# Kernel optimization log

Measured on AMD Instinct MI355X. Metric: run time of the kernel, lower is better.

## Reference

```python
import jax, jax.numpy as jnp
import numpy as np

OUT_F, IN_F = 8192, 4096
TOKENS = 512


def _unpack_int2_to_ternary(packed, alpha, dtype):
    # packed: [out_f, in_f//4] ints 0..255; 4 two-bit codes per byte.
    # code 0 -> -1, code 2 -> +1, codes 1/3 -> 0; then scale by per-row alpha.
    shifts = jnp.arange(4, dtype=packed.dtype) * 2  # [0,2,4,6]
    two_bit = (packed[:, :, None] >> shifts[None, None, :]) & 3  # [out_f, in_f//4, 4]
    two_bit = two_bit.reshape(packed.shape[0], -1)  # [out_f, in_f]
    sign = jnp.where(two_bit == 2, 1.0, jnp.where(two_bit == 0, -1.0, 0.0)).astype(dtype)
    return sign * alpha.astype(dtype)[:, None]


def setup_inputs() -> dict:
    key = jax.random.key(0)
    k1, k2, k3, k4 = jax.random.split(key, 4)
    x = jax.random.normal(k1, (TOKENS, IN_F), dtype=jnp.float32)
    weight_int2 = jax.random.randint(k2, (OUT_F, IN_F // 4), 0, 256, dtype=jnp.int32)
    alpha = jax.random.uniform(k3, (OUT_F,), dtype=jnp.float32, minval=0.01, maxval=0.05)
    bias = jax.random.normal(k4, (OUT_F,), dtype=jnp.float32) * 0.01
    return {"x": x, "weight_int2": weight_int2, "alpha": alpha, "bias": bias}


def reference(x, weight_int2, alpha, bias):
    W = _unpack_int2_to_ternary(weight_int2, alpha, x.dtype)  # [out_f, in_f]
    out = x @ W.T  # [tokens, out_f]
    return out + bias
```

## Files before the change

### kernel.cpp

```cpp
#include <hip/hip_runtime.h>
#include <hip/hip_bf16.h>

typedef unsigned int u32;
typedef unsigned short u16;

#define TOKENS 512
#define OUT_F  8192
#define IN_F   4096
#define KPACK  (IN_F / 4)
#define NSTEP  64

typedef __attribute__((ext_vector_type(8))) short bf16x8;
typedef __attribute__((ext_vector_type(4))) float f32x4;
typedef __attribute__((ext_vector_type(16))) float f32x16;

__device__ __forceinline__ u32 pack_bf16x2(float a, float b) {
    __hip_bfloat162 h = __float22bfloat162_rn(make_float2(a, b));
    union { __hip_bfloat162 h2; u32 u; } cvt;
    cvt.h2 = h;
    return cvt.u;
}

__device__ __forceinline__ void decode4(u32 b, u32& lo, u32& hi) {
    u32 t = b + (b << 14);
    u32 u = t >> 4;
    u32 nt = ~t, nu = ~u;
    lo = __umul24(nt & 0x10001u, 0x3F80u) | ((nt & 0x20002u) << 14);
    hi = __umul24(nu & 0x10001u, 0x3F80u) | ((nu & 0x20002u) << 14);
}

__device__ __forceinline__ bf16x8 decode_frag(u32 hw) {
    u32 d0, d1, d2, d3;
    decode4(hw & 0xFFu, d0, d1);
    decode4((hw >> 8) & 0xFFu, d2, d3);
    union { bf16x8 v; u32 u[4]; } c;
    c.u[0] = d0; c.u[1] = d1; c.u[2] = d2; c.u[3] = d3;
    return c.v;
}

__device__ __forceinline__ void async_ld16(const void* g, void* l) {
    __builtin_amdgcn_global_load_lds(
        (const __attribute__((address_space(1))) u32*)g,
        (__attribute__((address_space(3))) u32*)l, 16, 0, 0);
}

__global__ __launch_bounds__(256) void convert_x(const float* __restrict__ X,
                                                 u16* __restrict__ Xb) {
    int i = (blockIdx.x * 256 + threadIdx.x) * 8;
    float4 a = *(const float4*)(X + i);
    float4 b = *(const float4*)(X + i + 4);
    uint4 q;
    q.x = pack_bf16x2(a.x, a.y);
    q.y = pack_bf16x2(a.z, a.w);
    q.z = pack_bf16x2(b.x, b.y);
    q.w = pack_bf16x2(b.z, b.w);
    *(uint4*)(Xb + i) = q;
}

__global__ __launch_bounds__(256) void repack_w6(const u32* __restrict__ W2,
                                                 u32* __restrict__ W6) {
    __shared__ u32 staged[128 * 16];
    const int ngrp = blockIdx.x;
    const int kc   = blockIdx.y;
    const int t = threadIdx.x;

    {
        const int c = t & 15;
#pragma unroll
        for (int i = 0; i < 8; ++i) {
            int r = i * 16 + (t >> 4);
            uint4 w = *(const uint4*)(W2 + (size_t)(ngrp * 128 + r) * KPACK + kc * 64 + c * 4);
            staged[r * 16 + (c ^ (r & 15))] =
                (w.x & 0xFFu) | ((w.y & 0xFFu) << 8) | ((w.z & 0xFFu) << 16) | ((w.w & 0xFFu) << 24);
        }
    }
    __syncthreads();
    {
        const u16* sp = (const u16*)staged;
#pragma unroll
        for (int j = 0; j < 8; ++j) {
            int e = t + 256 * j;
            int lane = e & 63;
            int kq   = (e >> 6) & 3;
            int Sl   = (e >> 8) & 3;
            int nh   = (e >> 10) & 1;
            int hw = Sl * 8 + kq * 2 + (lane >> 5);
            int r0 = nh * 64 + (lane & 31);
            int r1 = r0 + 32;
            u32 x0 = sp[r0 * 32 + 2 * ((hw >> 1) ^ (r0 & 15)) + (hw & 1)];
            u32 x1 = sp[r1 * 32 + 2 * ((hw >> 1) ^ (r1 & 15)) + (hw & 1)];
            size_t idx = (size_t)(ngrp * 2 + nh) * 16384 + (size_t)(kc * 4 + Sl) * 256
                       + kq * 64 + lane;
            W6[idx] = x0 | (x1 << 16);
        }
    }
}

__global__ __launch_bounds__(512, 2) void ternary_gemm_ks(
    const u16* __restrict__ Xb,
    const u32* __restrict__ W6,
    const float* __restrict__ alpha,
    const float* __restrict__ bias,
    float* __restrict__ Out)
{
    __shared__ uint4 smem[4096];
    u16* As = (u16*)smem;

    const int tid  = threadIdx.x;
    const int lane = tid & 63;
    const int wave = tid >> 6;
    const int kq = wave & 3;
    const int nh = wave >> 2;

    const int m0 = blockIdx.x * 128;
    const int n0 = blockIdx.y * 128;
    const int ngrp = blockIdx.y;

    f32x16 acc[4][2];
#pragma unroll
    for (int mt = 0; mt < 4; ++mt)
#pragma unroll
        for (int nt = 0; nt < 2; ++nt)
#pragma unroll
            for (int i = 0; i < 16; ++i)
                acc[mt][nt][i] = 0.f;

    const int slot = ((kq * 2 + (lane >> 5)) ^ (lane & 7));
    int ofsA[4];
#pragma unroll
    for (int mt = 0; mt < 4; ++mt)
        ofsA[mt] = (mt * 32 + (lane & 31)) * 64 + slot * 8;

    const int r_l = lane >> 3;
    const int c_l = (lane & 7) ^ r_l;
    const u16* gA[2];
    u16* lA[2];
#pragma unroll
    for (int i = 0; i < 2; ++i) {
        int rbase = wave * 16 + i * 8;
        gA[i] = Xb + (size_t)(m0 + rbase + r_l) * IN_F + c_l * 8;
        lA[i] = As + rbase * 64;
    }

    const u32* wp = W6 + (size_t)(ngrp * 2 + nh) * 16384 + kq * 64 + lane;

    u32 wcur = wp[0];
    u32 wnxt = wp[256];
#pragma unroll
    for (int i = 0; i < 2; ++i) async_ld16(gA[i], lA[i]);
    __syncthreads();

    for (int s = 0; s < NSTEP; ++s) {
        const int buf = s & 1;
        if (s + 1 < NSTEP) {
            const int off = (s + 1) * 64;
#pragma unroll
            for (int i = 0; i < 2; ++i)
                async_ld16(gA[i] + off, lA[i] + (buf ^ 1) * 8192);
        }
        u32 wtmp = 0;
        if (s + 2 < NSTEP) wtmp = wp[(size_t)(s + 2) * 256];

        const u16* ab = As + buf * 8192;
        bf16x8 a0 = *(const bf16x8*)(ab + ofsA[0]);
        bf16x8 a1 = *(const bf16x8*)(ab + ofsA[1]);
        bf16x8 a2 = *(const bf16x8*)(ab + ofsA[2]);
        bf16x8 a3 = *(const bf16x8*)(ab + ofsA[3]);
        bf16x8 b0 = decode_frag(wcur & 0xFFFFu);
        bf16x8 b1 = decode_frag(wcur >> 16);

        acc[0][0] = __builtin_amdgcn_mfma_f32_32x32x16_bf16(a0, b0, acc[0][0], 0, 0, 0);
        acc[1][0] = __builtin_amdgcn_mfma_f32_32x32x16_bf16(a1, b0, acc[1][0], 0, 0, 0);
        acc[2][0] = __builtin_amdgcn_mfma_f32_32x32x16_bf16(a2, b0, acc[2][0], 0, 0, 0);
        acc[3][0] = __builtin_amdgcn_mfma_f32_32x32x16_bf16(a3, b0, acc[3][0], 0, 0, 0);
        acc[0][1] = __builtin_amdgcn_mfma_f32_32x32x16_bf16(a0, b1, acc[0][1], 0, 0, 0);
        acc[1][1] = __builtin_amdgcn_mfma_f32_32x32x16_bf16(a1, b1, acc[1][1], 0, 0, 0);
        acc[2][1] = __builtin_amdgcn_mfma_f32_32x32x16_bf16(a2, b1, acc[2][1], 0, 0, 0);
        acc[3][1] = __builtin_amdgcn_mfma_f32_32x32x16_bf16(a3, b1, acc[3][1], 0, 0, 0);

        wcur = wnxt;
        wnxt = wtmp;
        __syncthreads();
    }

    f32x4* red = (f32x4*)smem;
#pragma unroll 1
    for (int q = 1; q < 4; ++q) {
        if (kq == q) {
            f32x4* dst = red + nh * 2048 + lane;
#pragma unroll
            for (int mt = 0; mt < 4; ++mt)
#pragma unroll
                for (int nt = 0; nt < 2; ++nt)
#pragma unroll
                    for (int sub = 0; sub < 4; ++sub) {
                        f32x4 v = {acc[mt][nt][sub * 4 + 0], acc[mt][nt][sub * 4 + 1],
                                   acc[mt][nt][sub * 4 + 2], acc[mt][nt][sub * 4 + 3]};
                        dst[(mt * 8 + nt * 4 + sub) * 64] = v;
                    }
        }
        __syncthreads();
        if (kq == 0) {
            const f32x4* src = red + nh * 2048 + lane;
#pragma unroll
            for (int mt = 0; mt < 4; ++mt)
#pragma unroll
                for (int nt = 0; nt < 2; ++nt)
#pragma unroll
                    for (int sub = 0; sub < 4; ++sub) {
                        f32x4 v = src[(mt * 8 + nt * 4 + sub) * 64];
#pragma unroll
                        for (int i = 0; i < 4; ++i)
                            acc[mt][nt][sub * 4 + i] += v[i];
                    }
        }
        __syncthreads();
    }

    if (kq == 0) {
#pragma unroll
        for (int nt = 0; nt < 2; ++nt) {
            int ncol = n0 + nh * 64 + nt * 32 + (lane & 31);
            float av = alpha[ncol];
            float bv = bias[ncol];
#pragma unroll
            for (int mt = 0; mt < 4; ++mt) {
#pragma unroll
                for (int r = 0; r < 16; ++r) {
                    int row = m0 + mt * 32 + (r & 3) + 8 * (r >> 2) + 4 * (lane >> 5);
                    Out[(size_t)row * OUT_F + ncol] = acc[mt][nt][r] * av + bv;
                }
            }
        }
    }
}

__global__ void ternary_naive(const float* __restrict__ X, const u32* __restrict__ W2,
                              const float* __restrict__ alpha, const float* __restrict__ bias,
                              float* __restrict__ Out) {
    int o  = blockIdx.x * 64 + (threadIdx.x & 63);
    int tk = blockIdx.y * 4 + (threadIdx.x >> 6);
    const float* x = X + (size_t)tk * IN_F;
    const u32* w = W2 + (size_t)o * KPACK;
    float s = 0.f;
    for (int d = 0; d < KPACK; ++d) {
        u32 b = w[d] & 0xFFu;
        const float* xp = x + d * 4;
#pragma unroll
        for (int j = 0; j < 4; ++j) {
            u32 c = (b >> (2 * j)) & 3u;
            float wv = (c == 2u) ? 1.f : ((c == 0u) ? -1.f : 0.f);
            s += xp[j] * wv;
        }
    }
    Out[(size_t)tk * OUT_F + o] = s * alpha[o] + bias[o];
}

extern "C" void kernel_launch(void* const* d_in, const int* in_sizes, int n_in,
                              void* d_out, int out_size, void* d_ws, size_t ws_size,
                              hipStream_t stream) {
    const float* x = (const float*)d_in[0];
    const u32* w2 = (const u32*)d_in[1];
    const float* alpha = (const float*)d_in[2];
    const float* bias  = (const float*)d_in[3];
    float* out = (float*)d_out;

    const size_t xb_bytes = (size_t)TOKENS * IN_F * sizeof(u16);
    const size_t w6_bytes = (size_t)OUT_F * IN_F / 4;

    if (ws_size >= xb_bytes + w6_bytes) {
        u16* xb = (u16*)d_ws;
        u32* w6 = (u32*)((char*)d_ws + xb_bytes);
        convert_x<<<(TOKENS * IN_F) / (256 * 8), 256, 0, stream>>>(x, xb);
        repack_w6<<<dim3(64, 16), 256, 0, stream>>>(w2, w6);
        ternary_gemm_ks<<<dim3(4, 64), 512, 0, stream>>>(xb, w6, alpha, bias, out);
    } else {
        ternary_naive<<<dim3(OUT_F / 64, TOKENS / 4), 256, 0, stream>>>(x, w2, alpha, bias, out);
    }
}
```

Before: 137.6 us.

## Shrink M tile to 64, widen K window to 128, and use a cheaper perm-based ternary decode

Result: faster. 131.8 us (-4.2%).

```diff
diff --git a/kernel.cpp b/kernel.cpp
--- a/kernel.cpp
+++ b/kernel.cpp
@@ -8,7 +8,10 @@
 #define OUT_F  8192
 #define IN_F   4096
 #define KPACK  (IN_F / 4)
-#define NSTEP  64
+#define TM 64
+#define TN 128
+#define BKW 128
+#define NWIN (IN_F / BKW)
 
 typedef __attribute__((ext_vector_type(8))) short bf16x8;
 typedef __attribute__((ext_vector_type(4))) float f32x4;
@@ -21,20 +24,16 @@
     return cvt.u;
 }
 
-__device__ __forceinline__ void decode4(u32 b, u32& lo, u32& hi) {
-    u32 t = b + (b << 14);
-    u32 u = t >> 4;
-    u32 nt = ~t, nu = ~u;
-    lo = __umul24(nt & 0x10001u, 0x3F80u) | ((nt & 0x20002u) << 14);
-    hi = __umul24(nu & 0x10001u, 0x3F80u) | ((nu & 0x20002u) << 14);
-}
-
-__device__ __forceinline__ bf16x8 decode_frag(u32 hw) {
-    u32 d0, d1, d2, d3;
-    decode4(hw & 0xFFu, d0, d1);
-    decode4((hw >> 8) & 0xFFu, d2, d3);
+__device__ __forceinline__ u32 decode_pair(u32 d) {
+    u32 s = (__umul24(d, 0x808202u) & 0x06060606u) + 0x01000100u;
+    return __builtin_amdgcn_perm(0x00003F80u, 0x0000BF80u, s);
+}
+__device__ __forceinline__ bf16x8 decode_frag(u32 w, int sh) {
     union { bf16x8 v; u32 u[4]; } c;
-    c.u[0] = d0; c.u[1] = d1; c.u[2] = d2; c.u[3] = d3;
+    c.u[0] = decode_pair((w >> (sh + 0)) & 0xFu);
+    c.u[1] = decode_pair((w >> (sh + 4)) & 0xFu);
+    c.u[2] = decode_pair((w >> (sh + 8)) & 0xFu);
+    c.u[3] = decode_pair((w >> (sh + 12)) & 0xFu);
     return c.v;
 }
 
@@ -57,54 +56,52 @@
     *(uint4*)(Xb + i) = q;
 }
 
-__global__ __launch_bounds__(256) void repack_w6(const u32* __restrict__ W2,
-                                                 u32* __restrict__ W6) {
-    __shared__ u32 staged[128 * 16];
+__global__ __launch_bounds__(256) void repack_w7(const u32* __restrict__ W2,
+                                                 uint2* __restrict__ W7) {
+    __shared__ u32 dense[128 * 32];
     const int ngrp = blockIdx.x;
     const int kc   = blockIdx.y;
     const int t = threadIdx.x;
-
-    {
-        const int c = t & 15;
-#pragma unroll
-        for (int i = 0; i < 8; ++i) {
-            int r = i * 16 + (t >> 4);
-            uint4 w = *(const uint4*)(W2 + (size_t)(ngrp * 128 + r) * KPACK + kc * 64 + c * 4);
-            staged[r * 16 + (c ^ (r & 15))] =
-                (w.x & 0xFFu) | ((w.y & 0xFFu) << 8) | ((w.z & 0xFFu) << 16) | ((w.w & 0xFFu) << 24);
-        }
+#pragma unroll
+    for (int i = 0; i < 16; ++i) {
+        int id = t + 256 * i;
+        int col = id >> 5, jq = id & 31;
+        uint4 wv = *(const uint4*)(W2 + (size_t)(ngrp * 128 + col) * KPACK + kc * 128 + jq * 4);
+        dense[col * 32 + (jq ^ (col & 31))] =
+            (wv.x & 0xFFu) | ((wv.y & 0xFFu) << 8) | ((wv.z & 0xFFu) << 16) | ((wv.w & 0xFFu) << 24);
     }
     __syncthreads();
-    {
-        const u16* sp = (const u16*)staged;
-#pragma unroll
-        for (int j = 0; j < 8; ++j) {
-            int e = t + 256 * j;
-            int lane = e & 63;
-            int kq   = (e >> 6) & 3;
-            int Sl   = (e >> 8) & 3;
-            int nh   = (e >> 10) & 1;
-            int hw = Sl * 8 + kq * 2 + (lane >> 5);
-            int r0 = nh * 64 + (lane & 31);
-            int r1 = r0 + 32;
-            u32 x0 = sp[r0 * 32 + 2 * ((hw >> 1) ^ (r0 & 15)) + (hw & 1)];
-            u32 x1 = sp[r1 * 32 + 2 * ((hw >> 1) ^ (r1 & 15)) + (hw & 1)];
-            size_t idx = (size_t)(ngrp * 2 + nh) * 16384 + (size_t)(kc * 4 + Sl) * 256
-                       + kq * 64 + lane;
-            W6[idx] = x0 | (x1 << 16);
-        }
-    }
-}
-
-__global__ __launch_bounds__(512, 2) void ternary_gemm_ks(
+    const u16* sp = (const u16*)dense;
+#pragma unroll
+    for (int p = 0; p < 8; ++p) {
+        int e = t + 256 * p;
+        int lane = e & 63;
+        int kq = (e >> 6) & 3;
+        int wloc = (e >> 8) & 3;
+        int nh = (e >> 10) & 1;
+        int h = lane >> 5;
+        int c0 = nh * 64 + (lane & 31), c1 = c0 + 32;
+        int j0 = wloc * 8 + kq * 2;
+        u32 x0 = sp[((c0 * 32 + (j0 ^ (c0 & 31))) << 1) | h];
+        u32 x1 = sp[((c0 * 32 + ((j0 + 1) ^ (c0 & 31))) << 1) | h];
+        u32 y0 = sp[((c1 * 32 + (j0 ^ (c1 & 31))) << 1) | h];
+        u32 y1 = sp[((c1 * 32 + ((j0 + 1) ^ (c1 & 31))) << 1) | h];
+        uint2 o;
+        o.x = x0 | (x1 << 16);
+        o.y = y0 | (y1 << 16);
+        int w = kc * 4 + wloc;
+        W7[(((size_t)(ngrp * 2 + nh) * 32 + w) * 4 + kq) * 64 + lane] = o;
+    }
+}
+
+__global__ __launch_bounds__(512, 4) void ternary_gemm7(
     const u16* __restrict__ Xb,
-    const u32* __restrict__ W6,
+    const uint2* __restrict__ W7,
     const float* __restrict__ alpha,
     const float* __restrict__ bias,
     float* __restrict__ Out)
 {
-    __shared__ uint4 smem[4096];
-    u16* As = (u16*)smem;
+    __shared__ u16 As[2][TM * BKW];
 
     const int tid  = threadIdx.x;
     const int lane = tid & 63;
@@ -112,103 +109,103 @@
     const int kq = wave & 3;
     const int nh = wave >> 2;
 
-    const int m0 = blockIdx.x * 128;
-    const int n0 = blockIdx.y * 128;
-    const int ngrp = blockIdx.y;
-
-    f32x16 acc[4][2];
-#pragma unroll
-    for (int mt = 0; mt < 4; ++mt)
+    const int id = blockIdx.x;
+    const int m0 = (id & 7) * TM;
+    const int ngrp = id >> 3;
+    const int n0 = ngrp * TN;
+
+    f32x16 acc[2][2];
+#pragma unroll
+    for (int mt = 0; mt < 2; ++mt)
 #pragma unroll
         for (int nt = 0; nt < 2; ++nt)
 #pragma unroll
             for (int i = 0; i < 16; ++i)
                 acc[mt][nt][i] = 0.f;
 
-    const int slot = ((kq * 2 + (lane >> 5)) ^ (lane & 7));
-    int ofsA[4];
-#pragma unroll
-    for (int mt = 0; mt < 4; ++mt)
-        ofsA[mt] = (mt * 32 + (lane & 31)) * 64 + slot * 8;
-
-    const int r_l = lane >> 3;
-    const int c_l = (lane & 7) ^ r_l;
-    const u16* gA[2];
-    u16* lA[2];
+    const u16* ga[2];
+    u32 lbase[2];
 #pragma unroll
     for (int i = 0; i < 2; ++i) {
-        int rbase = wave * 16 + i * 8;
-        gA[i] = Xb + (size_t)(m0 + rbase + r_l) * IN_F + c_l * 8;
-        lA[i] = As + rbase * 64;
-    }
-
-    const u32* wp = W6 + (size_t)(ngrp * 2 + nh) * 16384 + kq * 64 + lane;
-
-    u32 wcur = wp[0];
-    u32 wnxt = wp[256];
-#pragma unroll
-    for (int i = 0; i < 2; ++i) async_ld16(gA[i], lA[i]);
+        int rbase = wave * 8 + i * 4;
+        int row = rbase + (lane >> 4);
+        int cd = (lane & 15) ^ (row & 15);
+        ga[i] = Xb + (size_t)(m0 + row) * IN_F + cd * 8;
+        lbase[i] = rbase * BKW;
+    }
+
+    int ofsA[2][2];
+#pragma unroll
+    for (int mt = 0; mt < 2; ++mt)
+#pragma unroll
+        for (int ks = 0; ks < 2; ++ks) {
+            int row = mt * 32 + (lane & 31);
+            int chunk = kq * 4 + ks * 2 + (lane >> 5);
+            ofsA[mt][ks] = row * BKW + (chunk ^ (row & 15)) * 8;
+        }
+
+    const uint2* wp = W7 + ((size_t)(ngrp * 2 + nh) * NWIN * 4 + kq) * 64 + lane;
+
+    uint2 wcur = wp[0];
+    uint2 wnext = wp[256];
+#pragma unroll
+    for (int i = 0; i < 2; ++i) async_ld16(ga[i], &As[0][lbase[i]]);
     __syncthreads();
 
-    for (int s = 0; s < NSTEP; ++s) {
-        const int buf = s & 1;
-        if (s + 1 < NSTEP) {
-            const int off = (s + 1) * 64;
+    for (int w = 0; w < NWIN; ++w) {
+        const int buf = w & 1;
+        if (w + 1 < NWIN) {
+            const int koff = (w + 1) * BKW;
 #pragma unroll
             for (int i = 0; i < 2; ++i)
-                async_ld16(gA[i] + off, lA[i] + (buf ^ 1) * 8192);
-        }
-        u32 wtmp = 0;
-        if (s + 2 < NSTEP) wtmp = wp[(size_t)(s + 2) * 256];
-
-        const u16* ab = As + buf * 8192;
-        bf16x8 a0 = *(const bf16x8*)(ab + ofsA[0]);
-        bf16x8 a1 = *(const bf16x8*)(ab + ofsA[1]);
-        bf16x8 a2 = *(const bf16x8*)(ab + ofsA[2]);
-        bf16x8 a3 = *(const bf16x8*)(ab + ofsA[3]);
-        bf16x8 b0 = decode_frag(wcur & 0xFFFFu);
-        bf16x8 b1 = decode_frag(wcur >> 16);
-
-        acc[0][0] = __builtin_amdgcn_mfma_f32_32x32x16_bf16(a0, b0, acc[0][0], 0, 0, 0);
-        acc[1][0] = __builtin_amdgcn_mfma_f32_32x32x16_bf16(a1, b0, acc[1][0], 0, 0, 0);
-        acc[2][0] = __builtin_amdgcn_mfma_f32_32x32x16_bf16(a2, b0, acc[2][0], 0, 0, 0);
-        acc[3][0] = __builtin_amdgcn_mfma_f32_32x32x16_bf16(a3, b0, acc[3][0], 0, 0, 0);
-        acc[0][1] = __builtin_amdgcn_mfma_f32_32x32x16_bf16(a0, b1, acc[0][1], 0, 0, 0);
-        acc[1][1] = __builtin_amdgcn_mfma_f32_32x32x16_bf16(a1, b1, acc[1][1], 0, 0, 0);
-        acc[2][1] = __builtin_amdgcn_mfma_f32_32x32x16_bf16(a2, b1, acc[2][1], 0, 0, 0);
-        acc[3][1] = __builtin_amdgcn_mfma_f32_32x32x16_bf16(a3, b1, acc[3][1], 0, 0, 0);
-
-        wcur = wnxt;
-        wnxt = wtmp;
+                async_ld16(ga[i] + koff, &As[buf ^ 1][lbase[i]]);
+        }
+        uint2 wnn = make_uint2(0, 0);
+        if (w + 2 < NWIN) wnn = wp[(size_t)(w + 2) * 256];
+
+        const u16* ab = As[buf];
+#pragma unroll
+        for (int ks = 0; ks < 2; ++ks) {
+            bf16x8 a0 = *(const bf16x8*)(ab + ofsA[0][ks]);
+            bf16x8 a1 = *(const bf16x8*)(ab + ofsA[1][ks]);
+            bf16x8 b0 = decode_frag(wcur.x, ks * 16);
+            bf16x8 b1 = decode_frag(wcur.y, ks * 16);
+            acc[0][0] = __builtin_amdgcn_mfma_f32_32x32x16_bf16(a0, b0, acc[0][0], 0, 0, 0);
+            acc[1][0] = __builtin_amdgcn_mfma_f32_32x32x16_bf16(a1, b0, acc[1][0], 0, 0, 0);
+            acc[0][1] = __builtin_amdgcn_mfma_f32_32x32x16_bf16(a0, b1, acc[0][1], 0, 0, 0);
+            acc[1][1] = __builtin_amdgcn_mfma_f32_32x32x16_bf16(a1, b1, acc[1][1], 0, 0, 0);
+        }
+        wcur = wnext;
+        wnext = wnn;
         __syncthreads();
     }
 
-    f32x4* red = (f32x4*)smem;
+    f32x4* red = (f32x4*)As;
 #pragma unroll 1
     for (int q = 1; q < 4; ++q) {
         if (kq == q) {
-            f32x4* dst = red + nh * 2048 + lane;
-#pragma unroll
-            for (int mt = 0; mt < 4; ++mt)
+            f32x4* dst = red + nh * 1024 + lane;
+#pragma unroll
+            for (int mt = 0; mt < 2; ++mt)
 #pragma unroll
                 for (int nt = 0; nt < 2; ++nt)
 #pragma unroll
                     for (int sub = 0; sub < 4; ++sub) {
                         f32x4 v = {acc[mt][nt][sub * 4 + 0], acc[mt][nt][sub * 4 + 1],
                                    acc[mt][nt][sub * 4 + 2], acc[mt][nt][sub * 4 + 3]};
-                        dst[(mt * 8 + nt * 4 + sub) * 64] = v;
+                        dst[((mt * 2 + nt) * 4 + sub) * 64] = v;
                     }
         }
         __syncthreads();
         if (kq == 0) {
-            const f32x4* src = red + nh * 2048 + lane;
-#pragma unroll
-            for (int mt = 0; mt < 4; ++mt)
+            const f32x4* src = red + nh * 1024 + lane;
+#pragma unroll
+            for (int mt = 0; mt < 2; ++mt)
 #pragma unroll
                 for (int nt = 0; nt < 2; ++nt)
 #pragma unroll
                     for (int sub = 0; sub < 4; ++sub) {
-                        f32x4 v = src[(mt * 8 + nt * 4 + sub) * 64];
+                        f32x4 v = src[((mt * 2 + nt) * 4 + sub) * 64];
 #pragma unroll
                         for (int i = 0; i < 4; ++i)
                             acc[mt][nt][sub * 4 + i] += v[i];
@@ -224,7 +221,7 @@
             float av = alpha[ncol];
             float bv = bias[ncol];
 #pragma unroll
-            for (int mt = 0; mt < 4; ++mt) {
+            for (int mt = 0; mt < 2; ++mt) {
 #pragma unroll
                 for (int r = 0; r < 16; ++r) {
                     int row = m0 + mt * 32 + (r & 3) + 8 * (r >> 2) + 4 * (lane >> 5);
@@ -266,14 +263,14 @@
     float* out = (float*)d_out;
 
     const size_t xb_bytes = (size_t)TOKENS * IN_F * sizeof(u16);
-    const size_t w6_bytes = (size_t)OUT_F * IN_F / 4;
-
-    if (ws_size >= xb_bytes + w6_bytes) {
+    const size_t w7_bytes = (size_t)OUT_F * IN_F / 4;
+
+    if (ws_size >= xb_bytes + w7_bytes) {
         u16* xb = (u16*)d_ws;
-        u32* w6 = (u32*)((char*)d_ws + xb_bytes);
+        uint2* w7 = (uint2*)((char*)d_ws + xb_bytes);
         convert_x<<<(TOKENS * IN_F) / (256 * 8), 256, 0, stream>>>(x, xb);
-        repack_w6<<<dim3(64, 16), 256, 0, stream>>>(w2, w6);
-        ternary_gemm_ks<<<dim3(4, 64), 512, 0, stream>>>(xb, w6, alpha, bias, out);
+        repack_w7<<<dim3(64, 8), 256, 0, stream>>>(w2, w7);
+        ternary_gemm7<<<512, 512, 0, stream>>>(xb, w7, alpha, bias, out);
     } else {
         ternary_naive<<<dim3(OUT_F / 64, TOKENS / 4), 256, 0, stream>>>(x, w2, alpha, bias, out);
     }
```
